# Performance work log

Measured on AMD Instinct MI355X. Metric: run time of the kernel, lower is better.

Reference implementation:

```python
import jax, jax.numpy as jnp
import numpy as np

K = 1024
D = 512
DECAY = 0.99


def setup_inputs() -> dict:
    key = jax.random.key(0)
    k1, k2, k3 = jax.random.split(key, 3)
    z_e_x = jax.random.normal(k1, (64, 256, D), dtype=jnp.float32)
    codebook = jax.random.normal(k2, (K, D), dtype=jnp.float32)
    ema_count = jnp.ones((K,), dtype=jnp.float32)
    ema_w = jax.random.normal(k3, (K, D), dtype=jnp.float32)
    return {"z_e_x": z_e_x, "codebook": codebook,
            "ema_count": ema_count, "ema_w": ema_w}


def reference(z_e_x, codebook, ema_count, ema_w):
    # --- vector quantization: nearest codebook entry (squared L2) ---
    flat = z_e_x.reshape(-1, D)                       # [N, D]
    cb_sqr = jnp.sum(codebook ** 2, axis=1)           # [K]
    in_sqr = jnp.sum(flat ** 2, axis=1, keepdims=True)  # [N, 1]
    distances = (cb_sqr[None, :] + in_sqr) - 2.0 * (flat @ codebook.T)  # [N, K]
    indices = jnp.argmin(distances, axis=1)           # [N] int

    # straight-through codes from current codebook
    z_q_x = codebook[indices].reshape(z_e_x.shape)

    # --- EMA codebook update (training branch) ---
    counts = jnp.zeros((K,), dtype=flat.dtype).at[indices].add(1.0)       # sum of one-hots
    new_ema_count = DECAY * ema_count + (1.0 - DECAY) * counts
    dw = jnp.zeros((K, D), dtype=flat.dtype).at[indices].add(flat)        # one_hot.T @ flat
    new_ema_w = DECAY * ema_w + (1.0 - DECAY) * dw
    new_embedding = new_ema_w / new_ema_count[:, None]

    # codes from the updated codebook
    z_q_x_bar = new_embedding[indices].reshape(z_e_x.shape)

    return (z_q_x, z_q_x_bar, new_embedding, new_ema_count, new_ema_w)
```

## Files before the change

kernel.cpp:

```cpp
#include <hip/hip_runtime.h>

typedef _Float16 half8  __attribute__((ext_vector_type(8)));
typedef _Float16 half4v __attribute__((ext_vector_type(4)));
typedef float    f32x4  __attribute__((ext_vector_type(4)));

constexpr int K_CODES = 1024;
constexpr int D_DIM   = 512;
constexpr float DECAY = 0.99f;
constexpr float OMD   = 0.01f;
constexpr float LO_SCALE = 2048.0f;
constexpr float INV_LO   = 1.0f / 2048.0f;

constexpr int BM = 128;
constexpr int BN = 128;
constexpr int BK = 32;
constexpr int NPART = K_CODES / BN;
constexpr int CHUNK = 32;

__global__ __launch_bounds__(256) void zero_kernel(float4* __restrict__ p, int n4) {
    int i = blockIdx.x * 256 + threadIdx.x;
    if (i < n4) p[i] = make_float4(0.f, 0.f, 0.f, 0.f);
}

__global__ __launch_bounds__(64) void cbsqr_kernel(const float* __restrict__ cb,
                                                   float* __restrict__ out,
                                                   float* __restrict__ counts) {
    int k = blockIdx.x;
    int lane = threadIdx.x;
    float s = 0.f;
    for (int d = lane; d < D_DIM; d += 64) {
        float v = cb[(size_t)k * D_DIM + d];
        s += v * v;
    }
    #pragma unroll
    for (int off = 32; off > 0; off >>= 1) s += __shfl_down(s, off);
    if (lane == 0) { out[k] = s; counts[k] = 0.f; }
}

__global__ __launch_bounds__(256)
void splitB_kernel(const float* __restrict__ cb,
                   _Float16* __restrict__ bh, _Float16* __restrict__ bl) {
    int i = blockIdx.x * 256 + threadIdx.x;
    f32x4 v = reinterpret_cast<const f32x4*>(cb)[i];
    half4v h, l;
    #pragma unroll
    for (int j = 0; j < 4; ++j) {
        _Float16 hh = (_Float16)v[j];
        h[j] = hh;
        l[j] = (_Float16)((v[j] - (float)hh) * LO_SCALE);
    }
    reinterpret_cast<half4v*>(bh)[i] = h;
    reinterpret_cast<half4v*>(bl)[i] = l;
}

__global__ __launch_bounds__(256, 2)
void argmin_mfma(const float* __restrict__ A,
                 const _Float16* __restrict__ Bh,
                 const _Float16* __restrict__ Bl,
                 const float* __restrict__ cbsqr,
                 float* __restrict__ pval,
                 int*   __restrict__ pidx) {
    __shared__ float    As[BM * BK];
    __shared__ _Float16 Bhs[BN * BK];
    __shared__ _Float16 Bls[BN * BK];
    __shared__ float    sv[2][BM];
    __shared__ int      si[2][BM];

    const int tid  = threadIdx.x;
    const int lane = tid & 63;
    const int wid  = tid >> 6;
    const int wr = wid >> 1, wc = wid & 1;
    const int lq = lane >> 4;
    const int lr = lane & 15;

    const int row0  = blockIdx.x * BM;
    const int cbase = blockIdx.y * BN;

    f32x4 acc_h[4][4], acc_c[4][4];
    #pragma unroll
    for (int m = 0; m < 4; ++m)
        #pragma unroll
        for (int n = 0; n < 4; ++n) {
            acc_h[m][n] = f32x4{0.f, 0.f, 0.f, 0.f};
            acc_c[m][n] = f32x4{0.f, 0.f, 0.f, 0.f};
        }

    for (int d0 = 0; d0 < D_DIM; d0 += BK) {
        #pragma unroll
        for (int it = 0; it < 4; ++it) {
            int p = it * 4096 + wid * 1024 + lane * 16;
            int row  = p >> 7;
            int cpos = (p >> 4) & 7;
            int sc   = cpos ^ (row & 7);
            const float* src = A + (size_t)(row0 + row) * D_DIM + d0 + sc * 4;
            __builtin_amdgcn_global_load_lds(
                (const __attribute__((address_space(1))) void*)src,
                (__attribute__((address_space(3))) void*)(As + it * 1024 + wid * 256),
                16, 0, 0);
        }
        #pragma unroll
        for (int it = 0; it < 2; ++it) {
            int p = it * 4096 + wid * 1024 + lane * 16;
            int row  = p >> 6;
            int cpos = (p >> 4) & 3;
            int sc   = cpos ^ ((row ^ (row >> 2)) & 3);
            size_t goff = (size_t)(cbase + row) * D_DIM + d0 + sc * 8;
            __builtin_amdgcn_global_load_lds(
                (const __attribute__((address_space(1))) void*)(Bh + goff),
                (__attribute__((address_space(3))) void*)(Bhs + it * 2048 + wid * 512),
                16, 0, 0);
            __builtin_amdgcn_global_load_lds(
                (const __attribute__((address_space(1))) void*)(Bl + goff),
                (__attribute__((address_space(3))) void*)(Bls + it * 2048 + wid * 512),
                16, 0, 0);
        }
        __syncthreads();

        half8 bh[4], bl[4];
        #pragma unroll
        for (int n = 0; n < 4; ++n) {
            int rB  = wc * 64 + n * 16 + lr;
            int pos = lq ^ ((rB ^ (rB >> 2)) & 3);
            bh[n] = *reinterpret_cast<const half8*>(&Bhs[rB * 32 + pos * 8]);
            bl[n] = *reinterpret_cast<const half8*>(&Bls[rB * 32 + pos * 8]);
        }
        #pragma unroll
        for (int m = 0; m < 4; ++m) {
            int rA = wr * 64 + m * 16 + lr;
            int p0 = (2 * lq)     ^ (rA & 7);
            int p1 = (2 * lq + 1) ^ (rA & 7);
            f32x4 a0 = *reinterpret_cast<const f32x4*>(&As[rA * 32 + p0 * 4]);
            f32x4 a1 = *reinterpret_cast<const f32x4*>(&As[rA * 32 + p1 * 4]);
            half8 ah, al;
            #pragma unroll
            for (int j = 0; j < 4; ++j) {
                _Float16 h = (_Float16)a0[j];
                ah[j] = h;
                al[j] = (_Float16)((a0[j] - (float)h) * LO_SCALE);
            }
            #pragma unroll
            for (int j = 0; j < 4; ++j) {
                _Float16 h = (_Float16)a1[j];
                ah[4 + j] = h;
                al[4 + j] = (_Float16)((a1[j] - (float)h) * LO_SCALE);
            }
            #pragma unroll
            for (int n = 0; n < 4; ++n) {
                acc_h[m][n] = __builtin_amdgcn_mfma_f32_16x16x32_f16(ah, bh[n], acc_h[m][n], 0, 0, 0);
                acc_c[m][n] = __builtin_amdgcn_mfma_f32_16x16x32_f16(ah, bl[n], acc_c[m][n], 0, 0, 0);
                acc_c[m][n] = __builtin_amdgcn_mfma_f32_16x16x32_f16(al, bh[n], acc_c[m][n], 0, 0, 0);
            }
        }
        __syncthreads();
    }

    float cs[4];
    #pragma unroll
    for (int n = 0; n < 4; ++n) cs[n] = cbsqr[cbase + wc * 64 + n * 16 + lr];

    #pragma unroll
    for (int m = 0; m < 4; ++m) {
        #pragma unroll
        for (int q = 0; q < 4; ++q) {
            float bv = 3.4e38f;
            int   bi = 0;
            #pragma unroll
            for (int n = 0; n < 4; ++n) {
                float d = cs[n] - 2.0f * acc_h[m][n][q] - (2.0f * INV_LO) * acc_c[m][n][q];
                int   c = cbase + wc * 64 + n * 16 + lr;
                if (d < bv) { bv = d; bi = c; }
            }
            #pragma unroll
            for (int off = 1; off < 16; off <<= 1) {
                float v2 = __shfl_xor(bv, off);
                int   i2 = __shfl_xor(bi, off);
                if (v2 < bv || (v2 == bv && i2 < bi)) { bv = v2; bi = i2; }
            }
            if (lr == 0) {
                int prow = wr * 64 + m * 16 + lq * 4 + q;
                sv[wc][prow] = bv;
                si[wc][prow] = bi;
            }
        }
    }
    __syncthreads();
    if (tid < BM) {
        float v0 = sv[0][tid], v1 = sv[1][tid];
        int   i0 = si[0][tid], i1 = si[1][tid];
        float bv = (v1 < v0) ? v1 : v0;
        int   bi = (v1 < v0) ? i1 : i0;
        pval[(size_t)(row0 + tid) * NPART + blockIdx.y] = bv;
        pidx[(size_t)(row0 + tid) * NPART + blockIdx.y] = bi;
    }
}

__global__ __launch_bounds__(256)
void combine_kernel(const float* __restrict__ pval, const int* __restrict__ pidx,
                    int* __restrict__ indices, float* __restrict__ counts, int N) {
    int r = blockIdx.x * 256 + threadIdx.x;
    if (r >= N) return;
    float bv = pval[(size_t)r * NPART];
    int   bi = pidx[(size_t)r * NPART];
    #pragma unroll
    for (int p = 1; p < NPART; ++p) {
        float v = pval[(size_t)r * NPART + p];
        int  ii = pidx[(size_t)r * NPART + p];
        if (v < bv) { bv = v; bi = ii; }
    }
    indices[r] = bi;
    atomicAdd(&counts[bi], 1.0f);
}

__global__ __launch_bounds__(256)
void scan_kernel(const float* __restrict__ counts,
                 int* __restrict__ offs, int* __restrict__ cursor) {
    __shared__ int part[256];
    int t = threadIdx.x;
    int c[4], s = 0;
    #pragma unroll
    for (int j = 0; j < 4; ++j) { c[j] = (int)counts[t * 4 + j]; s += c[j]; }
    part[t] = s;
    __syncthreads();
    for (int off = 1; off < 256; off <<= 1) {
        int v   = part[t];
        int add = (t >= off) ? part[t - off] : 0;
        __syncthreads();
        part[t] = v + add;
        __syncthreads();
    }
    int run = part[t] - s;
    #pragma unroll
    for (int j = 0; j < 4; ++j) {
        offs[t * 4 + j]   = run;
        cursor[t * 4 + j] = run;
        run += c[j];
    }
    if (t == 255) offs[K_CODES] = part[255];
}

__global__ __launch_bounds__(256)
void scatter_kernel(const int* __restrict__ indices, int* __restrict__ cursor,
                    int* __restrict__ packed, int N) {
    int r = blockIdx.x * 256 + threadIdx.x;
    if (r >= N) return;
    int k = indices[r];
    int pos = atomicAdd(&cursor[k], 1);
    packed[pos] = (k << 16) | r;
}

__global__ __launch_bounds__(128)
void chunksum_kernel(const float* __restrict__ flat, const int* __restrict__ packed,
                     float* __restrict__ dw, int N) {
    __shared__ int ent[CHUNK + 1];
    const int t = threadIdx.x;
    const int base = blockIdx.x * CHUNK;
    const int cnt = min(CHUNK, N - base);
    if (t < cnt) ent[t] = packed[base + t];
    if (t == cnt) ent[t] = -1;
    __syncthreads();

    f32x4 acc = {0.f, 0.f, 0.f, 0.f};
    for (int i0 = 0; i0 < cnt; i0 += 8) {
        const int m = min(8, cnt - i0);
        f32x4 v[8];
        #pragma unroll
        for (int j = 0; j < 8; ++j) {
            if (j < m) {
                int r = ent[i0 + j] & 0xFFFF;
                v[j] = *reinterpret_cast<const f32x4*>(&flat[(size_t)r * D_DIM + t * 4]);
            }
        }
        #pragma unroll
        for (int j = 0; j < 8; ++j) {
            if (j < m) {
                acc[0] += v[j][0]; acc[1] += v[j][1];
                acc[2] += v[j][2]; acc[3] += v[j][3];
                int k = ent[i0 + j] >> 16;
                if ((ent[i0 + j + 1] >> 16) != k) {
                    float* p = &dw[(size_t)k * D_DIM + t * 4];
                    atomicAdd(p + 0, acc[0]);
                    atomicAdd(p + 1, acc[1]);
                    atomicAdd(p + 2, acc[2]);
                    atomicAdd(p + 3, acc[3]);
                    acc = f32x4{0.f, 0.f, 0.f, 0.f};
                }
            }
        }
    }
}

__global__ __launch_bounds__(256)
void finalize_kernel(const float* __restrict__ ema_count, const float* __restrict__ ema_w,
                     const float* __restrict__ counts, const float* __restrict__ dw,
                     float* __restrict__ new_emb, float* __restrict__ new_count,
                     float* __restrict__ new_ema_w) {
    int gid = blockIdx.x * 256 + threadIdx.x;
    int k = gid >> 7;
    int d = (gid & 127) * 4;
    float nc = DECAY * ema_count[k] + OMD * counts[k];
    size_t off = (size_t)k * D_DIM + d;
    float4 w  = *reinterpret_cast<const float4*>(&ema_w[off]);
    float4 dv = *reinterpret_cast<const float4*>(&dw[off]);
    float4 nw;
    nw.x = DECAY * w.x + OMD * dv.x;
    nw.y = DECAY * w.y + OMD * dv.y;
    nw.z = DECAY * w.z + OMD * dv.z;
    nw.w = DECAY * w.w + OMD * dv.w;
    *reinterpret_cast<float4*>(&new_ema_w[off]) = nw;
    float inv = 1.0f / nc;
    float4 ne;
    ne.x = nw.x * inv; ne.y = nw.y * inv; ne.z = nw.z * inv; ne.w = nw.w * inv;
    *reinterpret_cast<float4*>(&new_emb[off]) = ne;
    if ((gid & 127) == 0) new_count[k] = nc;
}

__global__ __launch_bounds__(256)
void gather_kernel(const float* __restrict__ codebook, const float* __restrict__ new_emb,
                   const int* __restrict__ indices,
                   float* __restrict__ zq, float* __restrict__ zqb) {
    int gid = blockIdx.x * 256 + threadIdx.x;
    int r = gid >> 7;
    int d = (gid & 127) * 4;
    int k = indices[r];
    size_t src = (size_t)k * D_DIM + d;
    size_t dst = (size_t)r * D_DIM + d;
    *reinterpret_cast<float4*>(&zq[dst])  = *reinterpret_cast<const float4*>(&codebook[src]);
    *reinterpret_cast<float4*>(&zqb[dst]) = *reinterpret_cast<const float4*>(&new_emb[src]);
}

extern "C" void kernel_launch(void* const* d_in, const int* in_sizes, int n_in,
                              void* d_out, int out_size, void* d_ws, size_t ws_size,
                              hipStream_t stream) {
    const float* z_e_x     = (const float*)d_in[0];
    const float* codebook  = (const float*)d_in[1];
    const float* ema_count = (const float*)d_in[2];
    const float* ema_w     = (const float*)d_in[3];

    const int N = in_sizes[0] / D_DIM;

    float* out = (float*)d_out;
    float* z_q_x     = out;
    float* z_q_x_bar = z_q_x + (size_t)N * D_DIM;
    float* new_emb   = z_q_x_bar + (size_t)N * D_DIM;
    float* new_count = new_emb + (size_t)K_CODES * D_DIM;
    float* new_ema_w = new_count + K_CODES;

    char* ws = (char*)d_ws;
    int*   indices = (int*)ws;
    float* cbsqr   = (float*)(ws + (size_t)N * 4);
    float* pval    = cbsqr + K_CODES;
    int*   pidx    = (int*)(pval + (size_t)N * NPART);
    float* counts  = (float*)(pidx + (size_t)N * NPART);
    _Float16* bh   = (_Float16*)(counts + K_CODES);
    _Float16* bl   = bh + (size_t)K_CODES * D_DIM;
    float* dw      = (float*)bh;
    int*   offs    = (int*)(bl + (size_t)K_CODES * D_DIM);
    int*   cursor  = offs + K_CODES + 1;
    int*   packed  = cursor + K_CODES;

    cbsqr_kernel<<<K_CODES, 64, 0, stream>>>(codebook, cbsqr, counts);
    splitB_kernel<<<(K_CODES * D_DIM / 4) / 256, 256, 0, stream>>>(codebook, bh, bl);

    dim3 g_argmin(N / BM, K_CODES / BN);
    argmin_mfma<<<g_argmin, 256, 0, stream>>>(z_e_x, bh, bl, cbsqr, pval, pidx);

    combine_kernel<<<(N + 255) / 256, 256, 0, stream>>>(pval, pidx, indices, counts, N);

    scan_kernel<<<1, 256, 0, stream>>>(counts, offs, cursor);
    scatter_kernel<<<(N + 255) / 256, 256, 0, stream>>>(indices, cursor, packed, N);

    zero_kernel<<<(K_CODES * D_DIM / 4) / 256, 256, 0, stream>>>((float4*)dw, K_CODES * D_DIM / 4);
    chunksum_kernel<<<(N + CHUNK - 1) / CHUNK, 128, 0, stream>>>(z_e_x, packed, dw, N);

    finalize_kernel<<<(K_CODES * (D_DIM / 4)) / 256, 256, 0, stream>>>(
        ema_count, ema_w, counts, dw, new_emb, new_count, new_ema_w);

    gather_kernel<<<(N * (D_DIM / 4)) / 256, 256, 0, stream>>>(
        codebook, new_emb, indices, z_q_x, z_q_x_bar);
}
```

Measured before the change: 139.3 us.

## Pre-split activations into fp16 hi/lo buffers and fuse codebook prep kernels

Adds a pass that splits z_e_x into fp16 high and scaled-low halves once, storing them in the z_q_x_bar output region as scratch. The argmin GEMM then loads the fp16 halves directly instead of reconverting fp32 A tiles in every one of the 8 codebook-column blocks. The codebook squared-norm and codebook split kernels are merged into one launch. The cost is an extra full read and write of the activations and reliance on output memory being overwritten later by the gather kernel.

```diff
diff --git a/kernel.cpp b/kernel.cpp
--- a/kernel.cpp
+++ b/kernel.cpp
@@ -1,7 +1,6 @@
 #include <hip/hip_runtime.h>
 
 typedef _Float16 half8  __attribute__((ext_vector_type(8)));
-typedef _Float16 half4v __attribute__((ext_vector_type(4)));
 typedef float    f32x4  __attribute__((ext_vector_type(4)));
 
 constexpr int K_CODES = 1024;
@@ -22,45 +21,71 @@
     if (i < n4) p[i] = make_float4(0.f, 0.f, 0.f, 0.f);
 }
 
-__global__ __launch_bounds__(64) void cbsqr_kernel(const float* __restrict__ cb,
-                                                   float* __restrict__ out,
-                                                   float* __restrict__ counts) {
+__global__ __launch_bounds__(64)
+void prep_kernel(const float* __restrict__ cb, float* __restrict__ cbsqr,
+                 float* __restrict__ counts,
+                 _Float16* __restrict__ bh, _Float16* __restrict__ bl) {
     int k = blockIdx.x;
     int lane = threadIdx.x;
+    size_t base = (size_t)k * D_DIM + lane * 8;
+    f32x4 v0 = *reinterpret_cast<const f32x4*>(&cb[base]);
+    f32x4 v1 = *reinterpret_cast<const f32x4*>(&cb[base + 4]);
+    half8 h, l;
     float s = 0.f;
-    for (int d = lane; d < D_DIM; d += 64) {
-        float v = cb[(size_t)k * D_DIM + d];
-        s += v * v;
-    }
+    #pragma unroll
+    for (int j = 0; j < 4; ++j) {
+        s += v0[j] * v0[j];
+        _Float16 hh = (_Float16)v0[j];
+        h[j] = hh;
+        l[j] = (_Float16)((v0[j] - (float)hh) * LO_SCALE);
+    }
+    #pragma unroll
+    for (int j = 0; j < 4; ++j) {
+        s += v1[j] * v1[j];
+        _Float16 hh = (_Float16)v1[j];
+        h[4 + j] = hh;
+        l[4 + j] = (_Float16)((v1[j] - (float)hh) * LO_SCALE);
+    }
+    *reinterpret_cast<half8*>(&bh[base]) = h;
+    *reinterpret_cast<half8*>(&bl[base]) = l;
     #pragma unroll
     for (int off = 32; off > 0; off >>= 1) s += __shfl_down(s, off);
-    if (lane == 0) { out[k] = s; counts[k] = 0.f; }
-}
-
-__global__ __launch_bounds__(256)
-void splitB_kernel(const float* __restrict__ cb,
-                   _Float16* __restrict__ bh, _Float16* __restrict__ bl) {
-    int i = blockIdx.x * 256 + threadIdx.x;
-    f32x4 v = reinterpret_cast<const f32x4*>(cb)[i];
-    half4v h, l;
-    #pragma unroll
-    for (int j = 0; j < 4; ++j) {
-        _Float16 hh = (_Float16)v[j];
+    if (lane == 0) { cbsqr[k] = s; counts[k] = 0.f; }
+}
+
+__global__ __launch_bounds__(256)
+void splitA_kernel(const float* __restrict__ A,
+                   _Float16* __restrict__ ah, _Float16* __restrict__ al) {
+    size_t i8 = ((size_t)blockIdx.x * 256 + threadIdx.x) * 8;
+    f32x4 v0 = *reinterpret_cast<const f32x4*>(&A[i8]);
+    f32x4 v1 = *reinterpret_cast<const f32x4*>(&A[i8 + 4]);
+    half8 h, l;
+    #pragma unroll
+    for (int j = 0; j < 4; ++j) {
+        _Float16 hh = (_Float16)v0[j];
         h[j] = hh;
-        l[j] = (_Float16)((v[j] - (float)hh) * LO_SCALE);
-    }
-    reinterpret_cast<half4v*>(bh)[i] = h;
-    reinterpret_cast<half4v*>(bl)[i] = l;
+        l[j] = (_Float16)((v0[j] - (float)hh) * LO_SCALE);
+    }
+    #pragma unroll
+    for (int j = 0; j < 4; ++j) {
+        _Float16 hh = (_Float16)v1[j];
+        h[4 + j] = hh;
+        l[4 + j] = (_Float16)((v1[j] - (float)hh) * LO_SCALE);
+    }
+    *reinterpret_cast<half8*>(&ah[i8]) = h;
+    *reinterpret_cast<half8*>(&al[i8]) = l;
 }
 
 __global__ __launch_bounds__(256, 2)
-void argmin_mfma(const float* __restrict__ A,
+void argmin_mfma(const _Float16* __restrict__ Ah,
+                 const _Float16* __restrict__ Al,
                  const _Float16* __restrict__ Bh,
                  const _Float16* __restrict__ Bl,
                  const float* __restrict__ cbsqr,
                  float* __restrict__ pval,
                  int*   __restrict__ pidx) {
-    __shared__ float    As[BM * BK];
+    __shared__ _Float16 Ahs[BM * BK];
+    __shared__ _Float16 Als[BM * BK];
     __shared__ _Float16 Bhs[BN * BK];
     __shared__ _Float16 Bls[BN * BK];
     __shared__ float    sv[2][BM];
@@ -87,32 +112,26 @@
 
     for (int d0 = 0; d0 < D_DIM; d0 += BK) {
         #pragma unroll
-        for (int it = 0; it < 4; ++it) {
-            int p = it * 4096 + wid * 1024 + lane * 16;
-            int row  = p >> 7;
-            int cpos = (p >> 4) & 7;
-            int sc   = cpos ^ (row & 7);
-            const float* src = A + (size_t)(row0 + row) * D_DIM + d0 + sc * 4;
-            __builtin_amdgcn_global_load_lds(
-                (const __attribute__((address_space(1))) void*)src,
-                (__attribute__((address_space(3))) void*)(As + it * 1024 + wid * 256),
-                16, 0, 0);
-        }
-        #pragma unroll
         for (int it = 0; it < 2; ++it) {
             int p = it * 4096 + wid * 1024 + lane * 16;
             int row  = p >> 6;
             int cpos = (p >> 4) & 3;
             int sc   = cpos ^ ((row ^ (row >> 2)) & 3);
-            size_t goff = (size_t)(cbase + row) * D_DIM + d0 + sc * 8;
+            size_t aoff = (size_t)(row0 + row) * D_DIM + d0 + sc * 8;
+            size_t boff = (size_t)(cbase + row) * D_DIM + d0 + sc * 8;
+            int dst = it * 2048 + wid * 512;
             __builtin_amdgcn_global_load_lds(
-                (const __attribute__((address_space(1))) void*)(Bh + goff),
-                (__attribute__((address_space(3))) void*)(Bhs + it * 2048 + wid * 512),
-                16, 0, 0);
+                (const __attribute__((address_space(1))) void*)(Ah + aoff),
+                (__attribute__((address_space(3))) void*)(Ahs + dst), 16, 0, 0);
             __builtin_amdgcn_global_load_lds(
-                (const __attribute__((address_space(1))) void*)(Bl + goff),
-                (__attribute__((address_space(3))) void*)(Bls + it * 2048 + wid * 512),
-                16, 0, 0);
+                (const __attribute__((address_space(1))) void*)(Al + aoff),
+                (__attribute__((address_space(3))) void*)(Als + dst), 16, 0, 0);
+            __builtin_amdgcn_global_load_lds(
+                (const __attribute__((address_space(1))) void*)(Bh + boff),
+                (__attribute__((address_space(3))) void*)(Bhs + dst), 16, 0, 0);
+            __builtin_amdgcn_global_load_lds(
+                (const __attribute__((address_space(1))) void*)(Bl + boff),
+                (__attribute__((address_space(3))) void*)(Bls + dst), 16, 0, 0);
         }
         __syncthreads();
 
@@ -126,24 +145,10 @@
         }
         #pragma unroll
         for (int m = 0; m < 4; ++m) {
-            int rA = wr * 64 + m * 16 + lr;
-            int p0 = (2 * lq)     ^ (rA & 7);
-            int p1 = (2 * lq + 1) ^ (rA & 7);
-            f32x4 a0 = *reinterpret_cast<const f32x4*>(&As[rA * 32 + p0 * 4]);
-            f32x4 a1 = *reinterpret_cast<const f32x4*>(&As[rA * 32 + p1 * 4]);
-            half8 ah, al;
-            #pragma unroll
-            for (int j = 0; j < 4; ++j) {
-                _Float16 h = (_Float16)a0[j];
-                ah[j] = h;
-                al[j] = (_Float16)((a0[j] - (float)h) * LO_SCALE);
-            }
-            #pragma unroll
-            for (int j = 0; j < 4; ++j) {
-                _Float16 h = (_Float16)a1[j];
-                ah[4 + j] = h;
-                al[4 + j] = (_Float16)((a1[j] - (float)h) * LO_SCALE);
-            }
+            int rA  = wr * 64 + m * 16 + lr;
+            int pos = lq ^ ((rA ^ (rA >> 2)) & 3);
+            half8 ah = *reinterpret_cast<const half8*>(&Ahs[rA * 32 + pos * 8]);
+            half8 al = *reinterpret_cast<const half8*>(&Als[rA * 32 + pos * 8]);
             #pragma unroll
             for (int n = 0; n < 4; ++n) {
                 acc_h[m][n] = __builtin_amdgcn_mfma_f32_16x16x32_f16(ah, bh[n], acc_h[m][n], 0, 0, 0);
@@ -345,6 +350,9 @@
     float* new_count = new_emb + (size_t)K_CODES * D_DIM;
     float* new_ema_w = new_count + K_CODES;
 
+    _Float16* Ahs = (_Float16*)z_q_x_bar;
+    _Float16* Als = Ahs + (size_t)N * D_DIM;
+
     char* ws = (char*)d_ws;
     int*   indices = (int*)ws;
     float* cbsqr   = (float*)(ws + (size_t)N * 4);
@@ -358,11 +366,11 @@
     int*   cursor  = offs + K_CODES + 1;
     int*   packed  = cursor + K_CODES;
 
-    cbsqr_kernel<<<K_CODES, 64, 0, stream>>>(codebook, cbsqr, counts);
-    splitB_kernel<<<(K_CODES * D_DIM / 4) / 256, 256, 0, stream>>>(codebook, bh, bl);
+    prep_kernel<<<K_CODES, 64, 0, stream>>>(codebook, cbsqr, counts, bh, bl);
+    splitA_kernel<<<(N * D_DIM / 8) / 256, 256, 0, stream>>>(z_e_x, Ahs, Als);
 
     dim3 g_argmin(N / BM, K_CODES / BN);
-    argmin_mfma<<<g_argmin, 256, 0, stream>>>(z_e_x, bh, bl, cbsqr, pval, pidx);
+    argmin_mfma<<<g_argmin, 256, 0, stream>>>(Ahs, Als, bh, bl, cbsqr, pval, pidx);
 
     combine_kernel<<<(N + 255) / 256, 256, 0, stream>>>(pval, pidx, indices, counts, N);
 
```

After: 143.6 us. +3.1%, slower.
